# Kernel tuning notes

Measured on AMD Instinct MI355X. Metric: run time of the kernel, lower is better.

## Reference

```python
import jax, jax.numpy as jnp
import numpy as np

N, E, G = 200000, 600000, 1024
NF_IN, EF_IN, H = 32, 16, 512
BN_EPS = 1e-5


def _bn(x, gamma, beta):
    # eval-mode BatchNorm1d with running_mean=0, running_var=1
    return x * (gamma / jnp.sqrt(1.0 + BN_EPS)) + beta


def setup_inputs() -> dict:
    key = jax.random.key(0)
    ks = jax.random.split(key, 32)
    s = 0.05
    inp = {
        'nf': jax.random.normal(ks[0], (N, NF_IN), jnp.float32),
        'ef': jax.random.normal(ks[1], (E, EF_IN), jnp.float32),
        'gf': jax.random.normal(ks[2], (G, H), jnp.float32),
        'device_params': jax.random.uniform(ks[3], (N,), jnp.float32),
        'node_y': jax.random.randint(ks[4], (N,), 0, 9),
        'batch_idx': jnp.sort(jax.random.randint(ks[5], (N,), 0, G)),
        'edge_index': jax.random.randint(ks[6], (2, E), 0, N),
        'nf_w1': jax.random.normal(ks[7], (NF_IN + 9, H), jnp.float32) * s,
        'nf_b1': jax.random.normal(ks[8], (H,), jnp.float32) * s,
        'nf_g1': jax.random.uniform(ks[9], (H,), jnp.float32, 0.5, 1.5),
        'nf_be1': jax.random.normal(ks[10], (H,), jnp.float32) * s,
        'nf_w2': jax.random.normal(ks[11], (H, H), jnp.float32) * s,
        'nf_b2': jax.random.normal(ks[12], (H,), jnp.float32) * s,
        'ef_w1': jax.random.normal(ks[13], (EF_IN, H), jnp.float32) * s,
        'ef_b1': jax.random.normal(ks[14], (H,), jnp.float32) * s,
        'ef_g1': jax.random.uniform(ks[15], (H,), jnp.float32, 0.5, 1.5),
        'ef_be1': jax.random.normal(ks[16], (H,), jnp.float32) * s,
        'ef_w2': jax.random.normal(ks[17], (H, H), jnp.float32) * s,
        'ef_b2': jax.random.normal(ks[18], (H,), jnp.float32) * s,
        'ow1': jax.random.normal(ks[19], (H, H), jnp.float32) * s,
        'ob1': jax.random.normal(ks[20], (H,), jnp.float32) * s,
        'og1': jax.random.uniform(ks[21], (H,), jnp.float32, 0.5, 1.5),
        'obe1': jax.random.normal(ks[22], (H,), jnp.float32) * s,
        'ow2': jax.random.normal(ks[23], (H, H), jnp.float32) * s,
        'ob2': jax.random.normal(ks[24], (H,), jnp.float32) * s,
        'og2': jax.random.uniform(ks[25], (H,), jnp.float32, 0.5, 1.5),
        'obe2': jax.random.normal(ks[26], (H,), jnp.float32) * s,
        'ow3': jax.random.normal(ks[27], (H, 2), jnp.float32) * s,
        'ob3': jax.random.normal(ks[28], (2,), jnp.float32) * s,
    }
    return inp


def reference(nf, ef, gf, device_params, node_y, batch_idx, edge_index,
              nf_w1, nf_b1, nf_g1, nf_be1, nf_w2, nf_b2,
              ef_w1, ef_b1, ef_g1, ef_be1, ef_w2, ef_b2,
              ow1, ob1, og1, obe1, ow2, ob2, og2, obe2, ow3, ob3):
    num_graphs = gf.shape[0]
    gelu = lambda x: jax.nn.gelu(x, approximate=False)  # torch nn.GELU default

    # DeviceParam_MLP: augment node features with scaled one-hot of node class
    nf_aug = jnp.concatenate(
        [nf, jax.nn.one_hot(node_y, 9, dtype=nf.dtype) * device_params[:, None]],
        axis=-1)  # [N, nf_in+9]
    h_n = gelu(_bn(nf_aug @ nf_w1 + nf_b1, nf_g1, nf_be1)) @ nf_w2 + nf_b2  # [N,H]
    h_e = gelu(_bn(ef @ ef_w1 + ef_b1, ef_g1, ef_be1)) @ ef_w2 + ef_b2      # [E,H]

    # two scatter_add pools into graph features
    gh = gf
    gh = gh + jax.ops.segment_sum(h_n, batch_idx, num_segments=num_graphs)
    edge_graph = batch_idx[edge_index[0]]  # graph id of each edge's source node
    gh = gh + jax.ops.segment_sum(h_e, edge_graph, num_segments=num_graphs)

    # output MLP (layer_num=3): two hidden blocks + final Linear -> 2
    x = gelu(_bn(gh @ ow1 + ob1, og1, obe1))
    x = gelu(_bn(x @ ow2 + ob2, og2, obe2))
    return x @ ow3 + ob3  # [G, 2]
```

## Files before the change

### kernel.cpp

```cpp
#include <hip/hip_runtime.h>

#define NN 200000
#define NE 600000
#define NG 1024
#define HH 512

typedef short short8 __attribute__((ext_vector_type(8)));
typedef float f32x4 __attribute__((ext_vector_type(4)));

__device__ __forceinline__ unsigned short f2bf(float f){
  unsigned u = __float_as_uint(f);
  u += 0x7fffu + ((u >> 16) & 1u);
  return (unsigned short)(u >> 16);
}
__device__ __forceinline__ float bf2f(unsigned short h){
  return __uint_as_float(((unsigned)h) << 16);
}

__device__ __forceinline__ float gelu_f(float x){
  float p = __builtin_fmaf(x*x, -0.10294325f, -2.3022085f);
  float e = __builtin_amdgcn_exp2f(x * p);
  return x * __builtin_amdgcn_rcpf(1.0f + e);
}

__global__ __launch_bounds__(256) void kpre(
    const float* __restrict__ nfw1, const float* __restrict__ nfb1,
    const float* __restrict__ nfg1, const float* __restrict__ nfbe1,
    const float* __restrict__ efw1, const float* __restrict__ efb1,
    const float* __restrict__ efg1, const float* __restrict__ efbe1,
    unsigned short* __restrict__ w1nT, unsigned short* __restrict__ w1eT,
    float* __restrict__ b1n, float* __restrict__ b1e,
    const int* __restrict__ bidx, int* __restrict__ nstart,
    const int* __restrict__ eidx, int* __restrict__ eg, int* __restrict__ cnte){
  __shared__ int h[NG];
  const float rs = 0.99999500003750f;
  int b = blockIdx.x, t = threadIdx.x;
  if (b < 196){
    int tid = b*256 + t;
    if (tid < 512*64){
      int c = tid >> 6, k = tid & 63;
      float w = (k < 41) ? nfw1[k*HH + c] * nfg1[c] * rs : 0.0f;
      w1nT[tid] = f2bf(w);
    } else if (tid < 512*96){
      int u = tid - 512*64; int c = u >> 5, k = u & 31;
      float w = (k < 16) ? efw1[k*HH + c] * efg1[c] * rs : 0.0f;
      w1eT[u] = f2bf(w);
    } else if (tid < 512*96 + 512){
      int c = tid - 512*96;
      b1n[c] = nfb1[c]*nfg1[c]*rs + nfbe1[c];
    } else if (tid < 512*96 + 1024){
      int c = tid - (512*96 + 512);
      b1e[c] = efb1[c]*efg1[c]*rs + efbe1[c];
    }
  } else if (b < 978){
    int i = (b-196)*256 + t;
    if (i < NN){
      int g0 = bidx[i];
      int g1 = (i+1 < NN) ? bidx[i+1] : NG;
      for (int g = g0+1; g <= g1; ++g) nstart[g] = i+1;
      if (i == 0) for (int g = 0; g <= g0; ++g) nstart[g] = 0;
    }
  } else {
    int hb = b - 978;
    for (int u = t; u < NG; u += 256) h[u] = 0;
    __syncthreads();
    for (int e = hb*256 + t; e < NE; e += 256*256){
      int g = bidx[eidx[e]];
      eg[e] = g;
      atomicAdd(&h[g], 1);
    }
    __syncthreads();
    for (int u = t; u < NG; u += 256){ int c = h[u]; if (c) atomicAdd(&cnte[u], c); }
  }
}

__global__ __launch_bounds__(1024) void kscan_init(const int* __restrict__ cnte, int* __restrict__ cursor,
    int* __restrict__ estart,
    const float* __restrict__ gf, const int* __restrict__ nstart,
    const float* __restrict__ b2n, const float* __restrict__ b2e,
    float* __restrict__ gh){
  if (blockIdx.x == 0){
    __shared__ int s[NG];
    int t = threadIdx.x;
    int v = cnte[t]; s[t] = v; __syncthreads();
    for (int d = 1; d < NG; d <<= 1){
      int x = (t >= d) ? s[t-d] : 0;
      __syncthreads();
      s[t] += x;
      __syncthreads();
    }
    cursor[t] = s[t] - v;
    estart[t] = s[t] - v;
    if (t == NG-1) estart[NG] = s[t];
  } else {
    int i = (blockIdx.x - 1)*1024 + threadIdx.x;
    int f = i*4;
    int r = f >> 9, c = f & 511;
    float cn = (float)(nstart[r+1] - nstart[r]);
    float ce = (float)cnte[r];
    float4 gv = *(const float4*)&gf[f];
    float4 bn4 = *(const float4*)&b2n[c];
    float4 be4 = *(const float4*)&b2e[c];
    float4 o;
    o.x = gv.x + cn*bn4.x + ce*be4.x;
    o.y = gv.y + cn*bn4.y + ce*be4.y;
    o.z = gv.z + cn*bn4.z + ce*be4.z;
    o.w = gv.w + cn*bn4.w + ce*be4.w;
    *(float4*)&gh[f] = o;
  }
}

__global__ __launch_bounds__(1024) void kscatter(const int* __restrict__ eg, int* __restrict__ cursor,
                                                 int* __restrict__ perm){
  __shared__ int h[NG], base[NG];
  const int per = (NE + gridDim.x - 1) / gridDim.x;
  const int lo = blockIdx.x * per, hi = min(lo + per, NE);
  for (int t = threadIdx.x; t < NG; t += 1024) h[t] = 0;
  __syncthreads();
  for (int e = lo + threadIdx.x; e < hi; e += 1024) atomicAdd(&h[eg[e]], 1);
  __syncthreads();
  for (int t = threadIdx.x; t < NG; t += 1024){
    int c = h[t];
    base[t] = c ? atomicAdd(&cursor[t], c) : 0;
    h[t] = 0;
  }
  __syncthreads();
  for (int e = lo + threadIdx.x; e < hi; e += 1024){
    int g = eg[e];
    int p = base[g] + atomicAdd(&h[g], 1);
    perm[p] = e;
  }
}

__global__ __launch_bounds__(256) void kmain(
    const float* __restrict__ nf, const float* __restrict__ dp, const int* __restrict__ ny,
    const int* __restrict__ nstart, const float* __restrict__ ef, const int* __restrict__ perm,
    const int* __restrict__ estart, const unsigned short* __restrict__ w1nT,
    const unsigned short* __restrict__ w1eT, const float* __restrict__ b1n,
    const float* __restrict__ b1e, float* __restrict__ S){
  const int t = threadIdx.x;
  const int lane = t & 63, w = t >> 6;
  const int q = lane >> 4, m = lane & 15;
  const short8 zz = {0,0,0,0,0,0,0,0};
  if (blockIdx.x < 2048){
    const int g = blockIdx.x >> 1;
    const int c0 = ((blockIdx.x & 1) << 8) + (w << 6);
    short8 bfr[4]; float bias[4]; float colacc[4] = {0.f,0.f,0.f,0.f};
#pragma unroll
    for (int nt=0; nt<4; ++nt){
      int c = c0 + (nt<<4) + m;
      bfr[nt] = *(const short8*)(w1eT + (c << 5) + (q << 3));
      bias[nt] = b1e[c];
    }
    const int s0 = estart[g], s1 = estart[g+1];
    const int nfull = (s1 - s0) >> 4;
    int rb = s0;
    for (int ch=0; ch<nfull; ++ch, rb += 16){
      int e = perm[rb + m];
      short8 f = zz;
      if (q < 2){
        const float4* ap = (const float4*)(ef + (size_t)e*16 + (q<<3));
        float4 xa = ap[0], xb = ap[1];
        f[0]=(short)f2bf(xa.x); f[1]=(short)f2bf(xa.y); f[2]=(short)f2bf(xa.z); f[3]=(short)f2bf(xa.w);
        f[4]=(short)f2bf(xb.x); f[5]=(short)f2bf(xb.y); f[6]=(short)f2bf(xb.z); f[7]=(short)f2bf(xb.w);
      }
#pragma unroll
      for (int nt=0; nt<4; ++nt){
        f32x4 acc = {bias[nt], bias[nt], bias[nt], bias[nt]};
        acc = __builtin_amdgcn_mfma_f32_16x16x32_bf16(f, bfr[nt], acc, 0, 0, 0);
        colacc[nt] += (gelu_f(acc[0]) + gelu_f(acc[1])) + (gelu_f(acc[2]) + gelu_f(acc[3]));
      }
    }
    if (rb < s1){
      int row = rb + m;
      int e = perm[(row < s1) ? row : s0];
      short8 f = zz;
      if (q < 2){
        const float4* ap = (const float4*)(ef + (size_t)e*16 + (q<<3));
        float4 xa = ap[0], xb = ap[1];
        f[0]=(short)f2bf(xa.x); f[1]=(short)f2bf(xa.y); f[2]=(short)f2bf(xa.z); f[3]=(short)f2bf(xa.w);
        f[4]=(short)f2bf(xb.x); f[5]=(short)f2bf(xb.y); f[6]=(short)f2bf(xb.z); f[7]=(short)f2bf(xb.w);
      }
      const int vr = s1 - rb;
#pragma unroll
      for (int nt=0; nt<4; ++nt){
        f32x4 acc = {bias[nt], bias[nt], bias[nt], bias[nt]};
        acc = __builtin_amdgcn_mfma_f32_16x16x32_bf16(f, bfr[nt], acc, 0, 0, 0);
        float v0 = (q*4+0 < vr) ? gelu_f(acc[0]) : 0.f;
        float v1 = (q*4+1 < vr) ? gelu_f(acc[1]) : 0.f;
        float v2 = (q*4+2 < vr) ? gelu_f(acc[2]) : 0.f;
        float v3 = (q*4+3 < vr) ? gelu_f(acc[3]) : 0.f;
        colacc[nt] += (v0+v1)+(v2+v3);
      }
    }
#pragma unroll
    for (int nt=0; nt<4; ++nt){
      float s = colacc[nt];
      s += __shfl_xor(s, 16); s += __shfl_xor(s, 32);
      if (lane < 16) S[(size_t)g*1024 + 512 + c0 + (nt<<4) + lane] = s;
    }
  } else {
    const int b2 = blockIdx.x - 2048;
    const int g = b2 >> 2;
    const int c0 = ((b2 & 3) << 7) + (w << 5);
    short8 bf0[2], bf1[2]; float bias[2]; float colacc[2] = {0.f,0.f};
#pragma unroll
    for (int nt=0; nt<2; ++nt){
      int c = c0 + (nt<<4) + m;
      const short8* bp = (const short8*)(w1nT + (c << 6) + (q << 3));
      bf0[nt] = bp[0]; bf1[nt] = bp[4];
      bias[nt] = b1n[c];
    }
    const int s0 = nstart[g], s1 = nstart[g+1];
    const int nfull = (s1 - s0) >> 4;
    int rb = s0;
    for (int ch=0; ch<nfull; ++ch, rb += 16){
      int ar = rb + m;
      const float4* ap = (const float4*)(nf + (size_t)ar*32 + (q<<3));
      float4 xa = ap[0], xb = ap[1];
      short8 f;
      f[0]=(short)f2bf(xa.x); f[1]=(short)f2bf(xa.y); f[2]=(short)f2bf(xa.z); f[3]=(short)f2bf(xa.w);
      f[4]=(short)f2bf(xb.x); f[5]=(short)f2bf(xb.y); f[6]=(short)f2bf(xb.z); f[7]=(short)f2bf(xb.w);
      int cls = ny[ar];
      short dpb = (short)f2bf(dp[ar]);
      short8 h = zz;
      if (q == 0){
#pragma unroll
        for (int j=0;j<8;++j) h[j] = (cls==j) ? dpb : (short)0;
      } else if (q == 1 && cls == 8) h[0] = dpb;
#pragma unroll
      for (int nt=0; nt<2; ++nt){
        f32x4 acc = {bias[nt], bias[nt], bias[nt], bias[nt]};
        acc = __builtin_amdgcn_mfma_f32_16x16x32_bf16(f, bf0[nt], acc, 0, 0, 0);
        acc = __builtin_amdgcn_mfma_f32_16x16x32_bf16(h, bf1[nt], acc, 0, 0, 0);
        colacc[nt] += (gelu_f(acc[0]) + gelu_f(acc[1])) + (gelu_f(acc[2]) + gelu_f(acc[3]));
      }
    }
    if (rb < s1){
      int row = rb + m;
      int ar = (row < s1) ? row : s0;
      const float4* ap = (const float4*)(nf + (size_t)ar*32 + (q<<3));
      float4 xa = ap[0], xb = ap[1];
      short8 f;
      f[0]=(short)f2bf(xa.x); f[1]=(short)f2bf(xa.y); f[2]=(short)f2bf(xa.z); f[3]=(short)f2bf(xa.w);
      f[4]=(short)f2bf(xb.x); f[5]=(short)f2bf(xb.y); f[6]=(short)f2bf(xb.z); f[7]=(short)f2bf(xb.w);
      int cls = ny[ar];
      short dpb = (short)f2bf(dp[ar]);
      short8 h = zz;
      if (q == 0){
#pragma unroll
        for (int j=0;j<8;++j) h[j] = (cls==j) ? dpb : (short)0;
      } else if (q == 1 && cls == 8) h[0] = dpb;
      const int vr = s1 - rb;
#pragma unroll
      for (int nt=0; nt<2; ++nt){
        f32x4 acc = {bias[nt], bias[nt], bias[nt], bias[nt]};
        acc = __builtin_amdgcn_mfma_f32_16x16x32_bf16(f, bf0[nt], acc, 0, 0, 0);
        acc = __builtin_amdgcn_mfma_f32_16x16x32_bf16(h, bf1[nt], acc, 0, 0, 0);
        float v0 = (q*4+0 < vr) ? gelu_f(acc[0]) : 0.f;
        float v1 = (q*4+1 < vr) ? gelu_f(acc[1]) : 0.f;
        float v2 = (q*4+2 < vr) ? gelu_f(acc[2]) : 0.f;
        float v3 = (q*4+3 < vr) ? gelu_f(acc[3]) : 0.f;
        colacc[nt] += (v0+v1)+(v2+v3);
      }
    }
#pragma unroll
    for (int nt=0; nt<2; ++nt){
      float s = colacc[nt];
      s += __shfl_xor(s, 16); s += __shfl_xor(s, 32);
      if (lane < 16) S[(size_t)g*1024 + c0 + (nt<<4) + lane] = s;
    }
  }
}

__global__ __launch_bounds__(256) void kgemm3(const float* __restrict__ A, int lda, int nkc,
    const float* __restrict__ B0, const float* __restrict__ B1,
    float* __restrict__ out, const float* __restrict__ pre, const float* __restrict__ bias,
    const float* __restrict__ gam, const float* __restrict__ bet){
  const int t = threadIdx.x, lane = t & 63, w = t >> 6;
  const int q = lane >> 4, m = lane & 15;
  const int c0 = blockIdx.x*32, r0 = blockIdx.y*64 + w*16;
  f32x4 acc[2] = {{0.f,0.f,0.f,0.f},{0.f,0.f,0.f,0.f}};
  const float* ap = A + (size_t)(r0 + m)*lda + (q<<3);
  for (int kc = 0; kc < nkc; ++kc){
    const int ko = kc*32;
    float4 x = *(const float4*)(ap + ko);
    float4 y = *(const float4*)(ap + ko + 4);
    float v[8] = {x.x,x.y,x.z,x.w,y.x,y.y,y.z,y.w};
    short8 ah, al;
#pragma unroll
    for (int j=0;j<8;++j){
      unsigned short hh = f2bf(v[j]);
      ah[j] = (short)hh;
      al[j] = (short)f2bf(v[j] - bf2f(hh));
    }
    const float* Bp = (kc < 16) ? B0 : B1;
    const float* bp = Bp + (size_t)((kc & 15)*32 + (q<<3))*HH + c0 + m;
#pragma unroll
    for (int cf=0; cf<2; ++cf){
      float bv[8];
#pragma unroll
      for (int j=0;j<8;++j) bv[j] = bp[(size_t)j*HH + cf*16];
      short8 bh, bl;
#pragma unroll
      for (int j=0;j<8;++j){
        unsigned short hh = f2bf(bv[j]);
        bh[j] = (short)hh;
        bl[j] = (short)f2bf(bv[j] - bf2f(hh));
      }
      acc[cf] = __builtin_amdgcn_mfma_f32_16x16x32_bf16(ah, bh, acc[cf], 0, 0, 0);
      acc[cf] = __builtin_amdgcn_mfma_f32_16x16x32_bf16(ah, bl, acc[cf], 0, 0, 0);
      acc[cf] = __builtin_amdgcn_mfma_f32_16x16x32_bf16(al, bh, acc[cf], 0, 0, 0);
    }
  }
  const float rs = 0.99999500003750f;
#pragma unroll
  for (int cf=0; cf<2; ++cf){
    int c = c0 + cf*16 + m;
    float sc = 0.f, bi = 0.f, be = 0.f;
    if (!pre){ sc = gam[c]*rs; bi = bias[c]; be = bet[c]; }
#pragma unroll
    for (int i=0;i<4;++i){
      int r = blockIdx.y*64 + w*16 + q*4 + i;
      float vv = acc[cf][i];
      if (pre) vv += pre[(size_t)r*HH + c];
      else vv = gelu_f((vv + bi)*sc + be);
      out[(size_t)r*HH + c] = vv;
    }
  }
}

__global__ __launch_bounds__(256) void kfinal(const float* __restrict__ x2, const float* __restrict__ w3,
    const float* __restrict__ b3, float* __restrict__ out){
  const int lane = threadIdx.x & 63, wv = threadIdx.x >> 6;
  const int r = blockIdx.x*4 + wv;
  float a0 = 0.f, a1 = 0.f;
#pragma unroll
  for (int tt=0; tt<8; ++tt){
    int k = lane + tt*64;
    float x = x2[(size_t)r*HH + k];
    a0 = __builtin_fmaf(x, w3[2*k], a0);
    a1 = __builtin_fmaf(x, w3[2*k+1], a1);
  }
#pragma unroll
  for (int d=1; d<64; d<<=1){ a0 += __shfl_xor(a0, d); a1 += __shfl_xor(a1, d); }
  if (lane == 0){ out[r*2] = a0 + b3[0]; out[r*2+1] = a1 + b3[1]; }
}

extern "C" void kernel_launch(void* const* d_in, const int* in_sizes, int n_in,
                              void* d_out, int out_size, void* d_ws, size_t ws_size,
                              hipStream_t stream) {
  const float* nf    = (const float*)d_in[0];
  const float* ef    = (const float*)d_in[1];
  const float* gf    = (const float*)d_in[2];
  const float* dp    = (const float*)d_in[3];
  const int*   ny    = (const int*)d_in[4];
  const int*   bidx  = (const int*)d_in[5];
  const int*   eidx  = (const int*)d_in[6];
  const float* nfw1  = (const float*)d_in[7];
  const float* nfb1  = (const float*)d_in[8];
  const float* nfg1  = (const float*)d_in[9];
  const float* nfbe1 = (const float*)d_in[10];
  const float* w2n   = (const float*)d_in[11];
  const float* b2n   = (const float*)d_in[12];
  const float* efw1  = (const float*)d_in[13];
  const float* efb1  = (const float*)d_in[14];
  const float* efg1  = (const float*)d_in[15];
  const float* efbe1 = (const float*)d_in[16];
  const float* w2e   = (const float*)d_in[17];
  const float* b2e   = (const float*)d_in[18];
  const float* ow1   = (const float*)d_in[19];
  const float* ob1   = (const float*)d_in[20];
  const float* og1   = (const float*)d_in[21];
  const float* obe1  = (const float*)d_in[22];
  const float* ow2   = (const float*)d_in[23];
  const float* ob2   = (const float*)d_in[24];
  const float* og2   = (const float*)d_in[25];
  const float* obe2  = (const float*)d_in[26];
  const float* ow3   = (const float*)d_in[27];
  const float* ob3   = (const float*)d_in[28];

  float* S    = (float*)d_ws;
  int* cnte   = (int*)(S + NG*1024);
  int* cursor = cnte + NG;
  int* nstart = cursor + NG;
  int* estart = nstart + NG + 1;
  int* eg     = estart + NG + 1;
  int* perm   = eg + NE;
  unsigned short* w1nT = (unsigned short*)(perm + NE);
  unsigned short* w1eT = w1nT + HH*64;
  float* b1n  = (float*)(w1eT + HH*32);
  float* b1e  = b1n + HH;
  float* gh   = b1e + HH;
  float* xg2  = gh + NG*HH;
  float* x2f  = xg2 + NG*HH;

  hipMemsetAsync(cnte, 0, NG*sizeof(int), stream);

  kpre<<<1234, 256, 0, stream>>>(nfw1, nfb1, nfg1, nfbe1, efw1, efb1, efg1, efbe1,
                                 w1nT, w1eT, b1n, b1e, bidx, nstart, eidx, eg, cnte);
  kscan_init<<<129, 1024, 0, stream>>>(cnte, cursor, estart, gf, nstart, b2n, b2e, gh);
  kscatter<<<128, 1024, 0, stream>>>(eg, cursor, perm);
  kmain<<<6144, 256, 0, stream>>>(nf, dp, ny, nstart, ef, perm, estart,
                                  w1nT, w1eT, b1n, b1e, S);
  kgemm3<<<dim3(16,16), 256, 0, stream>>>(S, 1024, 32, w2n, w2e, gh, gh,
                                          nullptr, nullptr, nullptr);
  kgemm3<<<dim3(16,16), 256, 0, stream>>>(gh, 512, 16, ow1, ow1, xg2, nullptr,
                                          ob1, og1, obe1);
  kgemm3<<<dim3(16,16), 256, 0, stream>>>(xg2, 512, 16, ow2, ow2, x2f, nullptr,
                                          ob2, og2, obe2);
  kfinal<<<NG/4, 256, 0, stream>>>(x2f, ow3, ob3, (float*)d_out);
}
```

Baseline: 375.0 us.

## Fuse back-end GEMMs into cooperative kernel and drop memset via per-block histograms

Replaces the three back-end GEMM launches and the final projection with a single cooperative kernel that uses grid.sync between stages. The memset and the global atomic count are replaced by per-block histograms, which a single-block scan sums. The gh initialisation moves into the scatter kernel. Packed bf16 conversion intrinsics replace the manual rounding. The aim is to cut launch overhead and gaps between kernels, at the cost of grid-wide barriers and a serial 256-way sum in the scan.

```diff
diff --git a/kernel.cpp b/kernel.cpp
--- a/kernel.cpp
+++ b/kernel.cpp
@@ -1,4 +1,6 @@
 #include <hip/hip_runtime.h>
+#include <hip/hip_cooperative_groups.h>
+#include <hip/hip_bf16.h>
 
 #define NN 200000
 #define NE 600000
@@ -15,6 +17,28 @@
 }
 __device__ __forceinline__ float bf2f(unsigned short h){
   return __uint_as_float(((unsigned)h) << 16);
+}
+
+__device__ __forceinline__ short8 cvt8pk(float4 a, float4 b){
+  union { short8 s; __hip_bfloat162 h[4]; } u;
+  u.h[0] = __float22bfloat162_rn(make_float2(a.x, a.y));
+  u.h[1] = __float22bfloat162_rn(make_float2(a.z, a.w));
+  u.h[2] = __float22bfloat162_rn(make_float2(b.x, b.y));
+  u.h[3] = __float22bfloat162_rn(make_float2(b.z, b.w));
+  return u.s;
+}
+
+__device__ __forceinline__ void split8(const float* v, short8* hi, short8* lo){
+  union { short8 s; __hip_bfloat162 h[4]; unsigned u[4]; } H, L;
+#pragma unroll
+  for (int p=0;p<4;++p){
+    float a = v[2*p], b = v[2*p+1];
+    H.h[p] = __float22bfloat162_rn(make_float2(a, b));
+    unsigned hu = H.u[p];
+    L.h[p] = __float22bfloat162_rn(make_float2(a - __uint_as_float(hu << 16),
+                                               b - __uint_as_float(hu & 0xffff0000u)));
+  }
+  *hi = H.s; *lo = L.s;
 }
 
 __device__ __forceinline__ float gelu_f(float x){
@@ -31,7 +55,7 @@
     unsigned short* __restrict__ w1nT, unsigned short* __restrict__ w1eT,
     float* __restrict__ b1n, float* __restrict__ b1e,
     const int* __restrict__ bidx, int* __restrict__ nstart,
-    const int* __restrict__ eidx, int* __restrict__ eg, int* __restrict__ cnte){
+    const int* __restrict__ eidx, int* __restrict__ eg, int* __restrict__ hpart){
   __shared__ int h[NG];
   const float rs = 0.99999500003750f;
   int b = blockIdx.x, t = threadIdx.x;
@@ -70,48 +94,32 @@
       atomicAdd(&h[g], 1);
     }
     __syncthreads();
-    for (int u = t; u < NG; u += 256){ int c = h[u]; if (c) atomicAdd(&cnte[u], c); }
-  }
-}
-
-__global__ __launch_bounds__(1024) void kscan_init(const int* __restrict__ cnte, int* __restrict__ cursor,
-    int* __restrict__ estart,
-    const float* __restrict__ gf, const int* __restrict__ nstart,
-    const float* __restrict__ b2n, const float* __restrict__ b2e,
+    for (int u = t; u < NG; u += 256) hpart[hb*NG + u] = h[u];
+  }
+}
+
+__global__ __launch_bounds__(1024) void kscan(const int* __restrict__ hpart,
+    int* __restrict__ cursor, int* __restrict__ estart){
+  __shared__ int s[NG];
+  int t = threadIdx.x;
+  int v = 0;
+  for (int hb = 0; hb < 256; ++hb) v += hpart[hb*NG + t];
+  s[t] = v; __syncthreads();
+  for (int d = 1; d < NG; d <<= 1){
+    int x = (t >= d) ? s[t-d] : 0;
+    __syncthreads();
+    s[t] += x;
+    __syncthreads();
+  }
+  cursor[t] = s[t] - v;
+  estart[t] = s[t] - v;
+  if (t == NG-1) estart[NG] = s[t];
+}
+
+__global__ __launch_bounds__(1024) void kscatter(const int* __restrict__ eg, int* __restrict__ cursor,
+    int* __restrict__ perm, const int* __restrict__ estart, const int* __restrict__ nstart,
+    const float* __restrict__ gf, const float* __restrict__ b2n, const float* __restrict__ b2e,
     float* __restrict__ gh){
-  if (blockIdx.x == 0){
-    __shared__ int s[NG];
-    int t = threadIdx.x;
-    int v = cnte[t]; s[t] = v; __syncthreads();
-    for (int d = 1; d < NG; d <<= 1){
-      int x = (t >= d) ? s[t-d] : 0;
-      __syncthreads();
-      s[t] += x;
-      __syncthreads();
-    }
-    cursor[t] = s[t] - v;
-    estart[t] = s[t] - v;
-    if (t == NG-1) estart[NG] = s[t];
-  } else {
-    int i = (blockIdx.x - 1)*1024 + threadIdx.x;
-    int f = i*4;
-    int r = f >> 9, c = f & 511;
-    float cn = (float)(nstart[r+1] - nstart[r]);
-    float ce = (float)cnte[r];
-    float4 gv = *(const float4*)&gf[f];
-    float4 bn4 = *(const float4*)&b2n[c];
-    float4 be4 = *(const float4*)&b2e[c];
-    float4 o;
-    o.x = gv.x + cn*bn4.x + ce*be4.x;
-    o.y = gv.y + cn*bn4.y + ce*be4.y;
-    o.z = gv.z + cn*bn4.z + ce*be4.z;
-    o.w = gv.w + cn*bn4.w + ce*be4.w;
-    *(float4*)&gh[f] = o;
-  }
-}
-
-__global__ __launch_bounds__(1024) void kscatter(const int* __restrict__ eg, int* __restrict__ cursor,
-                                                 int* __restrict__ perm){
   __shared__ int h[NG], base[NG];
   const int per = (NE + gridDim.x - 1) / gridDim.x;
   const int lo = blockIdx.x * per, hi = min(lo + per, NE);
@@ -129,6 +137,22 @@
     int g = eg[e];
     int p = base[g] + atomicAdd(&h[g], 1);
     perm[p] = e;
+  }
+  {
+    int i = blockIdx.x*1024 + threadIdx.x;
+    int f = i*4;
+    int r = f >> 9, c = f & 511;
+    float cn = (float)(nstart[r+1] - nstart[r]);
+    float ce = (float)(estart[r+1] - estart[r]);
+    float4 gv = *(const float4*)&gf[f];
+    float4 bn4 = *(const float4*)&b2n[c];
+    float4 be4 = *(const float4*)&b2e[c];
+    float4 o;
+    o.x = gv.x + cn*bn4.x + ce*be4.x;
+    o.y = gv.y + cn*bn4.y + ce*be4.y;
+    o.z = gv.z + cn*bn4.z + ce*be4.z;
+    o.w = gv.w + cn*bn4.w + ce*be4.w;
+    *(float4*)&gh[f] = o;
   }
 }
 
@@ -160,9 +184,7 @@
       short8 f = zz;
       if (q < 2){
         const float4* ap = (const float4*)(ef + (size_t)e*16 + (q<<3));
-        float4 xa = ap[0], xb = ap[1];
-        f[0]=(short)f2bf(xa.x); f[1]=(short)f2bf(xa.y); f[2]=(short)f2bf(xa.z); f[3]=(short)f2bf(xa.w);
-        f[4]=(short)f2bf(xb.x); f[5]=(short)f2bf(xb.y); f[6]=(short)f2bf(xb.z); f[7]=(short)f2bf(xb.w);
+        f = cvt8pk(ap[0], ap[1]);
       }
 #pragma unroll
       for (int nt=0; nt<4; ++nt){
@@ -177,9 +199,7 @@
       short8 f = zz;
       if (q < 2){
         const float4* ap = (const float4*)(ef + (size_t)e*16 + (q<<3));
-        float4 xa = ap[0], xb = ap[1];
-        f[0]=(short)f2bf(xa.x); f[1]=(short)f2bf(xa.y); f[2]=(short)f2bf(xa.z); f[3]=(short)f2bf(xa.w);
-        f[4]=(short)f2bf(xb.x); f[5]=(short)f2bf(xb.y); f[6]=(short)f2bf(xb.z); f[7]=(short)f2bf(xb.w);
+        f = cvt8pk(ap[0], ap[1]);
       }
       const int vr = s1 - rb;
 #pragma unroll
@@ -217,10 +237,7 @@
     for (int ch=0; ch<nfull; ++ch, rb += 16){
       int ar = rb + m;
       const float4* ap = (const float4*)(nf + (size_t)ar*32 + (q<<3));
-      float4 xa = ap[0], xb = ap[1];
-      short8 f;
-      f[0]=(short)f2bf(xa.x); f[1]=(short)f2bf(xa.y); f[2]=(short)f2bf(xa.z); f[3]=(short)f2bf(xa.w);
-      f[4]=(short)f2bf(xb.x); f[5]=(short)f2bf(xb.y); f[6]=(short)f2bf(xb.z); f[7]=(short)f2bf(xb.w);
+      short8 f = cvt8pk(ap[0], ap[1]);
       int cls = ny[ar];
       short dpb = (short)f2bf(dp[ar]);
       short8 h = zz;
@@ -240,10 +257,7 @@
       int row = rb + m;
       int ar = (row < s1) ? row : s0;
       const float4* ap = (const float4*)(nf + (size_t)ar*32 + (q<<3));
-      float4 xa = ap[0], xb = ap[1];
-      short8 f;
-      f[0]=(short)f2bf(xa.x); f[1]=(short)f2bf(xa.y); f[2]=(short)f2bf(xa.z); f[3]=(short)f2bf(xa.w);
-      f[4]=(short)f2bf(xb.x); f[5]=(short)f2bf(xb.y); f[6]=(short)f2bf(xb.z); f[7]=(short)f2bf(xb.w);
+      short8 f = cvt8pk(ap[0], ap[1]);
       int cls = ny[ar];
       short dpb = (short)f2bf(dp[ar]);
       short8 h = zz;
@@ -273,13 +287,14 @@
   }
 }
 
-__global__ __launch_bounds__(256) void kgemm3(const float* __restrict__ A, int lda, int nkc,
+__device__ __forceinline__ void gemm_nolds(int cx, int ry,
+    const float* __restrict__ A, int lda, int nkc,
     const float* __restrict__ B0, const float* __restrict__ B1,
     float* __restrict__ out, const float* __restrict__ pre, const float* __restrict__ bias,
     const float* __restrict__ gam, const float* __restrict__ bet){
   const int t = threadIdx.x, lane = t & 63, w = t >> 6;
   const int q = lane >> 4, m = lane & 15;
-  const int c0 = blockIdx.x*32, r0 = blockIdx.y*64 + w*16;
+  const int c0 = cx*32, r0 = ry*64 + w*16;
   f32x4 acc[2] = {{0.f,0.f,0.f,0.f},{0.f,0.f,0.f,0.f}};
   const float* ap = A + (size_t)(r0 + m)*lda + (q<<3);
   for (int kc = 0; kc < nkc; ++kc){
@@ -288,12 +303,7 @@
     float4 y = *(const float4*)(ap + ko + 4);
     float v[8] = {x.x,x.y,x.z,x.w,y.x,y.y,y.z,y.w};
     short8 ah, al;
-#pragma unroll
-    for (int j=0;j<8;++j){
-      unsigned short hh = f2bf(v[j]);
-      ah[j] = (short)hh;
-      al[j] = (short)f2bf(v[j] - bf2f(hh));
-    }
+    split8(v, &ah, &al);
     const float* Bp = (kc < 16) ? B0 : B1;
     const float* bp = Bp + (size_t)((kc & 15)*32 + (q<<3))*HH + c0 + m;
 #pragma unroll
@@ -302,12 +312,7 @@
 #pragma unroll
       for (int j=0;j<8;++j) bv[j] = bp[(size_t)j*HH + cf*16];
       short8 bh, bl;
-#pragma unroll
-      for (int j=0;j<8;++j){
-        unsigned short hh = f2bf(bv[j]);
-        bh[j] = (short)hh;
-        bl[j] = (short)f2bf(bv[j] - bf2f(hh));
-      }
+      split8(bv, &bh, &bl);
       acc[cf] = __builtin_amdgcn_mfma_f32_16x16x32_bf16(ah, bh, acc[cf], 0, 0, 0);
       acc[cf] = __builtin_amdgcn_mfma_f32_16x16x32_bf16(ah, bl, acc[cf], 0, 0, 0);
       acc[cf] = __builtin_amdgcn_mfma_f32_16x16x32_bf16(al, bh, acc[cf], 0, 0, 0);
@@ -321,7 +326,7 @@
     if (!pre){ sc = gam[c]*rs; bi = bias[c]; be = bet[c]; }
 #pragma unroll
     for (int i=0;i<4;++i){
-      int r = blockIdx.y*64 + w*16 + q*4 + i;
+      int r = ry*64 + w*16 + q*4 + i;
       float vv = acc[cf][i];
       if (pre) vv += pre[(size_t)r*HH + c];
       else vv = gelu_f((vv + bi)*sc + be);
@@ -330,21 +335,35 @@
   }
 }
 
-__global__ __launch_bounds__(256) void kfinal(const float* __restrict__ x2, const float* __restrict__ w3,
-    const float* __restrict__ b3, float* __restrict__ out){
+__global__ __launch_bounds__(256) void kback(
+    const float* __restrict__ S, const float* __restrict__ w2n, const float* __restrict__ w2e,
+    float* __restrict__ gh,
+    const float* __restrict__ ow1, const float* __restrict__ ob1,
+    const float* __restrict__ og1, const float* __restrict__ obe1, float* __restrict__ xg2,
+    const float* __restrict__ ow2, const float* __restrict__ ob2,
+    const float* __restrict__ og2, const float* __restrict__ obe2, float* __restrict__ x2f,
+    const float* __restrict__ ow3, const float* __restrict__ ob3, float* __restrict__ out){
+  cooperative_groups::grid_group grid = cooperative_groups::this_grid();
+  const int cx = blockIdx.x & 15, ry = blockIdx.x >> 4;
+  gemm_nolds(cx, ry, S, 1024, 32, w2n, w2e, gh, gh, nullptr, nullptr, nullptr);
+  grid.sync();
+  gemm_nolds(cx, ry, gh, 512, 16, ow1, ow1, xg2, nullptr, ob1, og1, obe1);
+  grid.sync();
+  gemm_nolds(cx, ry, xg2, 512, 16, ow2, ow2, x2f, nullptr, ob2, og2, obe2);
+  grid.sync();
   const int lane = threadIdx.x & 63, wv = threadIdx.x >> 6;
   const int r = blockIdx.x*4 + wv;
   float a0 = 0.f, a1 = 0.f;
 #pragma unroll
   for (int tt=0; tt<8; ++tt){
     int k = lane + tt*64;
-    float x = x2[(size_t)r*HH + k];
-    a0 = __builtin_fmaf(x, w3[2*k], a0);
-    a1 = __builtin_fmaf(x, w3[2*k+1], a1);
+    float x = x2f[(size_t)r*HH + k];
+    a0 = __builtin_fmaf(x, ow3[2*k], a0);
+    a1 = __builtin_fmaf(x, ow3[2*k+1], a1);
   }
 #pragma unroll
   for (int d=1; d<64; d<<=1){ a0 += __shfl_xor(a0, d); a1 += __shfl_xor(a1, d); }
-  if (lane == 0){ out[r*2] = a0 + b3[0]; out[r*2+1] = a1 + b3[1]; }
+  if (lane == 0){ out[r*2] = a0 + ob3[0]; out[r*2+1] = a1 + ob3[1]; }
 }
 
 extern "C" void kernel_launch(void* const* d_in, const int* in_sizes, int n_in,
@@ -381,33 +400,30 @@
   const float* ob3   = (const float*)d_in[28];
 
   float* S    = (float*)d_ws;
-  int* cnte   = (int*)(S + NG*1024);
-  int* cursor = cnte + NG;
+  int* cursor = (int*)(S + NG*1024);
   int* nstart = cursor + NG;
   int* estart = nstart + NG + 1;
   int* eg     = estart + NG + 1;
   int* perm   = eg + NE;
-  unsigned short* w1nT = (unsigned short*)(perm + NE);
+  int* hpart  = perm + NE;
+  unsigned short* w1nT = (unsigned short*)(hpart + 256*NG);
   unsigned short* w1eT = w1nT + HH*64;
   float* b1n  = (float*)(w1eT + HH*32);
   float* b1e  = b1n + HH;
   float* gh   = b1e + HH;
   float* xg2  = gh + NG*HH;
   float* x2f  = xg2 + NG*HH;
-
-  hipMemsetAsync(cnte, 0, NG*sizeof(int), stream);
+  float* outf = (float*)d_out;
 
   kpre<<<1234, 256, 0, stream>>>(nfw1, nfb1, nfg1, nfbe1, efw1, efb1, efg1, efbe1,
-                                 w1nT, w1eT, b1n, b1e, bidx, nstart, eidx, eg, cnte);
-  kscan_init<<<129, 1024, 0, stream>>>(cnte, cursor, estart, gf, nstart, b2n, b2e, gh);
-  kscatter<<<128, 1024, 0, stream>>>(eg, cursor, perm);
+                                 w1nT, w1eT, b1n, b1e, bidx, nstart, eidx, eg, hpart);
+  kscan<<<1, 1024, 0, stream>>>(hpart, cursor, estart);
+  kscatter<<<128, 1024, 0, stream>>>(eg, cursor, perm, estart, nstart, gf, b2n, b2e, gh);
   kmain<<<6144, 256, 0, stream>>>(nf, dp, ny, nstart, ef, perm, estart,
                                   w1nT, w1eT, b1n, b1e, S);
-  kgemm3<<<dim3(16,16), 256, 0, stream>>>(S, 1024, 32, w2n, w2e, gh, gh,
-                                          nullptr, nullptr, nullptr);
-  kgemm3<<<dim3(16,16), 256, 0, stream>>>(gh, 512, 16, ow1, ow1, xg2, nullptr,
-                                          ob1, og1, obe1);
-  kgemm3<<<dim3(16,16), 256, 0, stream>>>(xg2, 512, 16, ow2, ow2, x2f, nullptr,
-                                          ob2, og2, obe2);
-  kfinal<<<NG/4, 256, 0, stream>>>(x2f, ow3, ob3, (float*)d_out);
-}
+  void* bargs[] = { (void*)&S, (void*)&w2n, (void*)&w2e, (void*)&gh,
+                    (void*)&ow1, (void*)&ob1, (void*)&og1, (void*)&obe1, (void*)&xg2,
+                    (void*)&ow2, (void*)&ob2, (void*)&og2, (void*)&obe2, (void*)&x2f,
+                    (void*)&ow3, (void*)&ob3, (void*)&outf };
+  hipLaunchCooperativeKernel((void*)kback, dim3(256), dim3(256), bargs, 0, stream);
+}
```

Result: slower. 512.4 us (+36.6%).
